# Optimization experiments

Hardware: AMD Instinct MI355X
Metric: run time of the kernel (lower is better)

Reference implementation:

```python
import jax, jax.numpy as jnp
import numpy as np

D_MODEL = 1024
NUM_HEADS = 16

def _dense_params(key, d_in, d_out):
    kw, _ = jax.random.split(key)
    # flax default: lecun_normal kernel, zeros bias
    W = jax.random.normal(kw, (d_in, d_out), dtype=jnp.float32) / np.sqrt(d_in)
    b = jnp.zeros((d_out,), dtype=jnp.float32)
    return W, b

def setup_inputs() -> dict:
    key = jax.random.key(0)
    ks = jax.random.split(key, 8)
    B, Tx, Tc = 2, 2048, 2048
    x = jax.random.normal(ks[0], (B, Tx, D_MODEL), dtype=jnp.float32)
    context = jax.random.normal(ks[1], (B, Tc, D_MODEL), dtype=jnp.float32)
    Wq, bq = _dense_params(ks[2], D_MODEL, D_MODEL)
    Wks, bks = _dense_params(ks[3], D_MODEL, D_MODEL)
    Wvs, bvs = _dense_params(ks[4], D_MODEL, D_MODEL)
    Wkc, bkc = _dense_params(ks[5], D_MODEL, D_MODEL)
    Wvc, bvc = _dense_params(ks[6], D_MODEL, D_MODEL)
    Wo, bo = _dense_params(ks[7], D_MODEL, D_MODEL)
    return {"x": x, "context": context,
            "Wq": Wq, "bq": bq, "Wks": Wks, "bks": bks, "Wvs": Wvs, "bvs": bvs,
            "Wkc": Wkc, "bkc": bkc, "Wvc": Wvc, "bvc": bvc, "Wo": Wo, "bo": bo}

def _split_heads(t, H):
    B, T, C = t.shape
    return t.reshape(B, T, H, C // H).transpose(0, 2, 1, 3)  # [B,H,T,hd]

def reference(x, context, Wq, bq, Wks, bks, Wvs, bvs, Wkc, bkc, Wvc, bvc, Wo, bo):
    H = NUM_HEADS
    head_dim = D_MODEL // H
    q = x @ Wq + bq
    k = jnp.concatenate([x @ Wks + bks, context @ Wkc + bkc], axis=1)
    v = jnp.concatenate([x @ Wvs + bvs, context @ Wvc + bvc], axis=1)
    q = _split_heads(q, H)  # [B,H,Tq,hd]
    k = _split_heads(k, H)  # [B,H,Tk,hd]
    v = _split_heads(v, H)
    attn = jnp.einsum('bhqd,bhkd->bhqk', q, k) / jnp.sqrt(jnp.float32(head_dim))
    attn = jax.nn.softmax(attn, axis=-1)
    out = jnp.einsum('bhqk,bhkd->bhqd', attn, v)
    B, _, Tq, _ = out.shape
    out = out.transpose(0, 2, 1, 3).reshape(B, Tq, D_MODEL)
    return out @ Wo + bo
```

## Files before the change

### kernel.cpp

```cpp
#include <hip/hip_runtime.h>
#include <hip/hip_bf16.h>
#include <math.h>


typedef _Float16 f16;
typedef _Float16 f16x8 __attribute__((ext_vector_type(8)));
typedef _Float16 f16x4v __attribute__((ext_vector_type(4)));
typedef float    f32x4 __attribute__((ext_vector_type(4)));

#define MFMA_F16(a, b, c) __builtin_amdgcn_mfma_f32_16x16x32_f16((a), (b), (c), 0, 0, 0)

#define QSCALE 0.18033688011112042f

__device__ __forceinline__ void glds16(const f16* g, f16* l) {
    __builtin_amdgcn_global_load_lds(
        (const __attribute__((address_space(1))) void*)g,
        (__attribute__((address_space(3))) void*)l, 16, 0, 0);
}

__global__ __launch_bounds__(256) void convert_xc(
    const float4* __restrict__ x, const float4* __restrict__ ctx,
    f16x4v* __restrict__ xb, f16x4v* __restrict__ cb)
{
    const int n4 = (2 * 2048 * 1024) / 4;
    int i = blockIdx.x * 256 + threadIdx.x;
    float4 v;
    f16x4v* dst;
    if (i < n4) { v = x[i];        dst = xb + i; }
    else        { v = ctx[i - n4]; dst = cb + (i - n4); }
    f16x4v h = { (f16)v.x, (f16)v.y, (f16)v.z, (f16)v.w };
    *dst = h;
}

__global__ __launch_bounds__(256) void pack_w(
    const float* __restrict__ W0, const float* __restrict__ W1,
    const float* __restrict__ W2, const float* __restrict__ W3,
    const float* __restrict__ W4, const float* __restrict__ W5,
    f16* __restrict__ out)
{
    const float* Ws[6] = { W0, W1, W2, W3, W4, W5 };
    const float* W = Ws[blockIdx.z];
    f16* Wt = out + (size_t)blockIdx.z * (1024 * 1024);

    __shared__ float tile[32][33];
    const int tx = threadIdx.x & 31, ty = threadIdx.x >> 5;
    const int n0 = blockIdx.x * 32, k0 = blockIdx.y * 32;

#pragma unroll
    for (int i = 0; i < 4; ++i) {
        int r = i * 8 + ty;
        tile[r][tx] = W[(size_t)(k0 + r) * 1024 + n0 + tx];
    }
    __syncthreads();
#pragma unroll
    for (int i = 0; i < 4; ++i) {
        int r = i * 8 + ty;
        Wt[(size_t)(n0 + r) * 1024 + k0 + tx] = (f16)tile[tx][r];
    }
}

#define GEMM_PROLOGUE(BN)                                                     \
    const int m0 = blockIdx.x * 128, n0 = blockIdx.y * (BN);                  \
    const int tid = threadIdx.x;                                              \
    const int w = tid >> 6, lane = tid & 63, quad = lane >> 4, l15 = lane & 15;\
    const int wm = (w >> 1) * 64, wn = (w & 1) * ((BN) / 2);                  \
    const int qsw = (quad ^ ((l15 >> 1) & 3)) * 8;                            \
    int gA[2], gB[(BN) / 64];                                                 \
    _Pragma("unroll")                                                         \
    for (int p = 0; p < 2; ++p) {                                             \
        int s = tid + p * 256;                                                \
        int r = (s >> 2) & 127, c = (s & 3) ^ ((s >> 3) & 3);                 \
        gA[p] = (m0 + r) * 1024 + c * 8;                                      \
    }                                                                         \
    _Pragma("unroll")                                                         \
    for (int p = 0; p < (BN) / 64; ++p) {                                     \
        int s = tid + p * 256;                                                \
        int r = (s >> 2) & ((BN) - 1), c = (s & 3) ^ ((s >> 3) & 3);          \
        gB[p] = (n0 + r) * 1024 + c * 8;                                      \
    }

#define GEMM_STAGE(BN)                                                        \
    __syncthreads();                                                          \
    _Pragma("unroll")                                                         \
    for (int p = 0; p < 2; ++p) glds16(&A[gA[p] + k0], &As[(p * 256 + w * 64) * 8]); \
    _Pragma("unroll")                                                         \
    for (int p = 0; p < (BN) / 64; ++p) glds16(&Bt[gB[p] + k0], &Bs[(p * 256 + w * 64) * 8]); \
    __syncthreads();

__global__ __launch_bounds__(256) void qk_gemm(
    const f16* __restrict__ xb, const f16* __restrict__ cb,
    const f16* __restrict__ wt,
    const float* __restrict__ bq, const float* __restrict__ bks,
    const float* __restrict__ bkc,
    f16* __restrict__ qbuf, f16* __restrict__ kbuf)
{
    __shared__ alignas(16) f16 As[128 * 32];
    __shared__ alignas(16) f16 Bs[128 * 32];

    const int z = blockIdx.z;
    const f16* A = (z == 2) ? cb : xb;
    const f16* Bt = wt + (size_t)(z == 0 ? 0 : (z == 1 ? 1 : 3)) * 1048576;
    const float* bias = (z == 0) ? bq : (z == 1) ? bks : bkc;
    const int roff = (z == 2) ? 2048 : 0;

    GEMM_PROLOGUE(128)
    f32x4 acc[4][4] = {};

    for (int k0 = 0; k0 < 1024; k0 += 32) {
        GEMM_STAGE(128)
        f16x8 a[4], b[4];
#pragma unroll
        for (int i = 0; i < 4; ++i)
            a[i] = *(const f16x8*)&As[(wm + i * 16 + l15) * 32 + qsw];
#pragma unroll
        for (int i = 0; i < 4; ++i)
            b[i] = *(const f16x8*)&Bs[(wn + i * 16 + l15) * 32 + qsw];
#pragma unroll
        for (int mi = 0; mi < 4; ++mi)
#pragma unroll
            for (int ni = 0; ni < 4; ++ni)
                acc[mi][ni] = MFMA_F16(a[mi], b[ni], acc[mi][ni]);
    }

#pragma unroll
    for (int mi = 0; mi < 4; ++mi) {
#pragma unroll
        for (int r = 0; r < 4; ++r) {
            int row = m0 + wm + mi * 16 + quad * 4 + r;
            int b_ = row >> 11, tok = row & 2047;
#pragma unroll
            for (int ni = 0; ni < 4; ++ni) {
                int col = n0 + wn + ni * 16 + l15;
                float v = acc[mi][ni][r] + bias[col];
                int bh = b_ * 16 + (col >> 6);
                if (z == 0) {
                    qbuf[((size_t)bh * 2048 + tok) * 64 + (col & 63)] = (f16)(v * QSCALE);
                } else {
                    int tg = roff + tok;
                    kbuf[(size_t)bh * 262144 + (size_t)(tg >> 6) * 4096
                         + (size_t)((col >> 5) & 1) * 2048 + (tg & 63) * 32 + (col & 31)] = (f16)v;
                }
            }
        }
    }
}

__global__ __launch_bounds__(256) void v_gemm(
    const f16* __restrict__ xb, const f16* __restrict__ cb,
    const f16* __restrict__ wt,
    const float* __restrict__ bvs, const float* __restrict__ bvc,
    f16* __restrict__ vt)
{
    __shared__ alignas(16) f16 As[128 * 32];
    __shared__ alignas(16) f16 Bs[128 * 32];

    const int z = blockIdx.z;
    const f16* A = z ? cb : xb;
    const f16* Bt = wt + (size_t)(z ? 4 : 2) * 1048576;
    const float* bias = z ? bvc : bvs;
    const int roff = z ? 2048 : 0;

    GEMM_PROLOGUE(128)
    f32x4 acc[4][4] = {};

    for (int k0 = 0; k0 < 1024; k0 += 32) {
        GEMM_STAGE(128)
        f16x8 a[4], b[4];
#pragma unroll
        for (int i = 0; i < 4; ++i)
            a[i] = *(const f16x8*)&As[(wm + i * 16 + l15) * 32 + qsw];
#pragma unroll
        for (int i = 0; i < 4; ++i)
            b[i] = *(const f16x8*)&Bs[(wn + i * 16 + l15) * 32 + qsw];
#pragma unroll
        for (int mi = 0; mi < 4; ++mi)
#pragma unroll
            for (int ni = 0; ni < 4; ++ni)
                acc[mi][ni] = MFMA_F16(b[ni], a[mi], acc[mi][ni]);
    }

#pragma unroll
    for (int mi = 0; mi < 4; ++mi) {
        int tok = m0 + wm + mi * 16 + l15;
        int b_ = tok >> 11;
        int tg = roff + (tok & 2047);
        size_t tbase = (size_t)(tg >> 6) * 4096 + (size_t)((tg >> 5) & 1) * 2048 + (tg & 31);
#pragma unroll
        for (int ni = 0; ni < 4; ++ni) {
#pragma unroll
            for (int r = 0; r < 4; ++r) {
                int wcol = n0 + wn + ni * 16 + quad * 4 + r;
                float v = acc[mi][ni][r] + bias[wcol];
                int bh = b_ * 16 + (wcol >> 6);
                vt[(size_t)bh * 262144 + tbase + (size_t)(wcol & 63) * 32] = (f16)v;
            }
        }
    }
}

__global__ __launch_bounds__(256) void out_gemm(
    const f16* __restrict__ abuf, const f16* __restrict__ wt5,
    const float* __restrict__ bo, float* __restrict__ out)
{
    __shared__ alignas(16) f16 As[128 * 32];
    __shared__ alignas(16) f16 Bs[64 * 32];

    const f16* A = abuf;
    const f16* Bt = wt5;

    GEMM_PROLOGUE(64)
    f32x4 acc[4][2] = {};

    for (int k0 = 0; k0 < 1024; k0 += 32) {
        GEMM_STAGE(64)
        f16x8 a[4], b[2];
#pragma unroll
        for (int i = 0; i < 4; ++i)
            a[i] = *(const f16x8*)&As[(wm + i * 16 + l15) * 32 + qsw];
#pragma unroll
        for (int i = 0; i < 2; ++i)
            b[i] = *(const f16x8*)&Bs[(wn + i * 16 + l15) * 32 + qsw];
#pragma unroll
        for (int mi = 0; mi < 4; ++mi)
#pragma unroll
            for (int ni = 0; ni < 2; ++ni)
                acc[mi][ni] = MFMA_F16(a[mi], b[ni], acc[mi][ni]);
    }

#pragma unroll
    for (int mi = 0; mi < 4; ++mi) {
#pragma unroll
        for (int r = 0; r < 4; ++r) {
            int row = m0 + wm + mi * 16 + quad * 4 + r;
#pragma unroll
            for (int ni = 0; ni < 2; ++ni) {
                int col = n0 + wn + ni * 16 + l15;
                out[(size_t)row * 1024 + col] = acc[mi][ni][r] + bo[col];
            }
        }
    }
}

__global__ __launch_bounds__(256, 2) void attn_kernel(
    const f16* __restrict__ q, const f16* __restrict__ kb,
    const f16* __restrict__ vtb, f16* __restrict__ o)
{
    __shared__ alignas(16) f16 K_lds[2][4096];
    __shared__ alignas(16) f16 V_lds[2][4096];
    __shared__ alignas(16) f16 P_lds[128 * 72];

    const int tid = threadIdx.x;
    const int w = tid >> 6, lane = tid & 63, quad = lane >> 4, l15 = lane & 15;
    const int bh = blockIdx.x, qt = blockIdx.y;
    const int b = bh >> 4, h = bh & 15;
    const int qbase = qt * 128;

    f16x8 qa[2][2];
#pragma unroll
    for (int nq = 0; nq < 2; ++nq) {
        const size_t qaddr =
            ((size_t)bh * 2048 + qbase + w * 32 + nq * 16 + l15) * 64 + quad * 8;
        qa[nq][0] = *(const f16x8*)&q[qaddr];
        qa[nq][1] = *(const f16x8*)&q[qaddr + 32];
    }

    f16x8 ones;
#pragma unroll
    for (int j = 0; j < 8; ++j) ones[j] = (f16)1.0f;

    f32x4 o_acc[2][4] = {};
    f32x4 l_acc[2] = {};

    const f16* ktile = kb + (size_t)bh * 262144;
    const f16* vtile = vtb + (size_t)bh * 262144;

    const int sco = ((tid >> 2) * 4 + ((tid & 3) ^ ((tid >> 3) & 3))) * 8;
    const int qsw = (quad ^ ((l15 >> 1) & 3)) * 8;
    const int wslot = w * 512;

    glds16(ktile + sco,        &K_lds[0][wslot]);
    glds16(ktile + 2048 + sco, &K_lds[0][2048 + wslot]);
    glds16(vtile + sco,        &V_lds[0][wslot]);
    glds16(vtile + 2048 + sco, &V_lds[0][2048 + wslot]);

    for (int kt = 0; kt < 64; ++kt) {
        const f16* Kc = K_lds[kt & 1];
        const f16* Vc = V_lds[kt & 1];
        f16* Kn = K_lds[(kt + 1) & 1];
        f16* Vn = V_lds[(kt + 1) & 1];

        __syncthreads();

        ktile += 4096; vtile += 4096;
        glds16(ktile + sco,        Kn + wslot);
        glds16(ktile + 2048 + sco, Kn + 2048 + wslot);
        glds16(vtile + sco,        Vn + wslot);
        glds16(vtile + 2048 + sco, Vn + 2048 + wslot);

        f32x4 s[4][2];
#pragma unroll
        for (int mt = 0; mt < 4; ++mt) {
            f16x8 ka0 = *(const f16x8*)&Kc[(mt * 16 + l15) * 32 + qsw];
            f16x8 ka1 = *(const f16x8*)&Kc[2048 + (mt * 16 + l15) * 32 + qsw];
#pragma unroll
            for (int nq = 0; nq < 2; ++nq) {
                f32x4 t = {};
                t = MFMA_F16(ka0, qa[nq][0], t);
                t = MFMA_F16(ka1, qa[nq][1], t);
                s[mt][nq] = t;
            }
        }

#pragma unroll
        for (int mt = 0; mt < 4; ++mt) {
#pragma unroll
            for (int nq = 0; nq < 2; ++nq) {
                f16x4v pk;
#pragma unroll
                for (int r = 0; r < 4; ++r)
                    pk[r] = (f16)__builtin_amdgcn_exp2f(s[mt][nq][r]);
                *(f16x4v*)&P_lds[(w * 32 + nq * 16 + l15) * 72 + mt * 16 + quad * 4] = pk;
            }
        }

        f16x8 pa[2][2];
#pragma unroll
        for (int nq = 0; nq < 2; ++nq)
#pragma unroll
            for (int ks = 0; ks < 2; ++ks)
                pa[nq][ks] = *(const f16x8*)&P_lds[(w * 32 + nq * 16 + l15) * 72 + ks * 32 + quad * 8];

#pragma unroll
        for (int nq = 0; nq < 2; ++nq) {
            l_acc[nq] = MFMA_F16(ones, pa[nq][0], l_acc[nq]);
            l_acc[nq] = MFMA_F16(ones, pa[nq][1], l_acc[nq]);
        }

#pragma unroll
        for (int dt = 0; dt < 4; ++dt) {
            f16x8 vb0 = *(const f16x8*)&Vc[(dt * 16 + l15) * 32 + qsw];
            f16x8 vb1 = *(const f16x8*)&Vc[2048 + (dt * 16 + l15) * 32 + qsw];
#pragma unroll
            for (int nq = 0; nq < 2; ++nq) {
                o_acc[nq][dt] = MFMA_F16(pa[nq][0], vb0, o_acc[nq][dt]);
                o_acc[nq][dt] = MFMA_F16(pa[nq][1], vb1, o_acc[nq][dt]);
            }
        }
    }

#pragma unroll
    for (int nq = 0; nq < 2; ++nq) {
#pragma unroll
        for (int r = 0; r < 4; ++r) {
            float lr = __shfl(l_acc[nq][0], quad * 4 + r, 64);
            float inv = 1.0f / lr;
            int ql = w * 32 + nq * 16 + quad * 4 + r;
            size_t obase = ((size_t)(b * 2048 + qbase + ql)) * 1024 + h * 64;
#pragma unroll
            for (int dt = 0; dt < 4; ++dt)
                o[obase + dt * 16 + l15] = (f16)(o_acc[nq][dt][r] * inv);
        }
    }
}

extern "C" void kernel_launch(void* const* d_in, const int* in_sizes, int n_in,
                              void* d_out, int out_size, void* d_ws, size_t ws_size,
                              hipStream_t stream)
{
    (void)in_sizes; (void)n_in; (void)out_size; (void)ws_size;

    const float* x    = (const float*)d_in[0];
    const float* ctx  = (const float*)d_in[1];
    const float* Wq   = (const float*)d_in[2];  const float* bq  = (const float*)d_in[3];
    const float* Wks  = (const float*)d_in[4];  const float* bks = (const float*)d_in[5];
    const float* Wvs  = (const float*)d_in[6];  const float* bvs = (const float*)d_in[7];
    const float* Wkc  = (const float*)d_in[8];  const float* bkc = (const float*)d_in[9];
    const float* Wvc  = (const float*)d_in[10]; const float* bvc = (const float*)d_in[11];
    const float* Wo   = (const float*)d_in[12]; const float* bo  = (const float*)d_in[13];

    char* ws = (char*)d_ws;
    f16* xb   = (f16*)(ws + 0);
    f16* cb   = (f16*)(ws + 8388608);
    f16* wt   = (f16*)(ws + 16777216);
    f16* qbuf = (f16*)(ws + 29360128);
    f16* kbuf = (f16*)(ws + 37748736);
    f16* vt   = (f16*)(ws + 54525952);
    f16* abuf = (f16*)(ws + 71303168);

    convert_xc<<<8192, 256, 0, stream>>>((const float4*)x, (const float4*)ctx,
                                         (f16x4v*)xb, (f16x4v*)cb);
    pack_w<<<dim3(32, 32, 6), 256, 0, stream>>>(Wq, Wks, Wvs, Wkc, Wvc, Wo, wt);

    qk_gemm<<<dim3(32, 8, 3), 256, 0, stream>>>(xb, cb, wt, bq, bks, bkc, qbuf, kbuf);
    v_gemm<<<dim3(32, 8, 2), 256, 0, stream>>>(xb, cb, wt, bvs, bvc, vt);

    attn_kernel<<<dim3(32, 16), 256, 0, stream>>>(qbuf, kbuf, vt, abuf);

    out_gemm<<<dim3(32, 16), 256, 0, stream>>>(abuf, wt + 5 * 1048576, bo, (float*)d_out);
}
```

Baseline: 317.8 us.

## Merge prep and projection kernels, add V transpose pass, widen attention waves

Fuses the input conversion and weight packing into one launch, and folds the Q/K and V projections into a single five-slice GEMM launch. V is now written row-major and transposed into the attention layout by a separate pass, reusing the xb workspace. The attention kernel drops to 128 threads per block, with each wave handling 64 queries instead of 32, which doubles register accumulators per wave and halves the number of waves. This trades launch count and occupancy for more K/V reuse per wave, at the cost of an extra V transpose kernel and higher register pressure.

After: 362.6 us. +14.1%, slower.

```diff
diff --git a/kernel.cpp b/kernel.cpp
--- a/kernel.cpp
+++ b/kernel.cpp
@@ -18,33 +18,34 @@
         (__attribute__((address_space(3))) void*)l, 16, 0, 0);
 }
 
-__global__ __launch_bounds__(256) void convert_xc(
+__global__ __launch_bounds__(256) void prep(
     const float4* __restrict__ x, const float4* __restrict__ ctx,
-    f16x4v* __restrict__ xb, f16x4v* __restrict__ cb)
-{
-    const int n4 = (2 * 2048 * 1024) / 4;
-    int i = blockIdx.x * 256 + threadIdx.x;
-    float4 v;
-    f16x4v* dst;
-    if (i < n4) { v = x[i];        dst = xb + i; }
-    else        { v = ctx[i - n4]; dst = cb + (i - n4); }
-    f16x4v h = { (f16)v.x, (f16)v.y, (f16)v.z, (f16)v.w };
-    *dst = h;
-}
-
-__global__ __launch_bounds__(256) void pack_w(
+    f16x4v* __restrict__ xb, f16x4v* __restrict__ cb,
     const float* __restrict__ W0, const float* __restrict__ W1,
     const float* __restrict__ W2, const float* __restrict__ W3,
     const float* __restrict__ W4, const float* __restrict__ W5,
-    f16* __restrict__ out)
-{
+    f16* __restrict__ wt)
+{
+    if (blockIdx.x < 8192) {
+        const int n4 = (2 * 2048 * 1024) / 4;
+        int i = blockIdx.x * 256 + threadIdx.x;
+        float4 v;
+        f16x4v* dst;
+        if (i < n4) { v = x[i];        dst = xb + i; }
+        else        { v = ctx[i - n4]; dst = cb + (i - n4); }
+        f16x4v h = { (f16)v.x, (f16)v.y, (f16)v.z, (f16)v.w };
+        *dst = h;
+        return;
+    }
+    const int idx = blockIdx.x - 8192;
+    const int z = idx >> 10, rem = idx & 1023;
     const float* Ws[6] = { W0, W1, W2, W3, W4, W5 };
-    const float* W = Ws[blockIdx.z];
-    f16* Wt = out + (size_t)blockIdx.z * (1024 * 1024);
+    const float* W = Ws[z];
+    f16* Wt = wt + (size_t)z * (1024 * 1024);
 
     __shared__ float tile[32][33];
     const int tx = threadIdx.x & 31, ty = threadIdx.x >> 5;
-    const int n0 = blockIdx.x * 32, k0 = blockIdx.y * 32;
+    const int n0 = (rem & 31) * 32, k0 = (rem >> 5) * 32;
 
 #pragma unroll
     for (int i = 0; i < 4; ++i) {
@@ -87,21 +88,24 @@
     for (int p = 0; p < (BN) / 64; ++p) glds16(&Bt[gB[p] + k0], &Bs[(p * 256 + w * 64) * 8]); \
     __syncthreads();
 
-__global__ __launch_bounds__(256) void qk_gemm(
+__global__ __launch_bounds__(256) void proj_gemm(
     const f16* __restrict__ xb, const f16* __restrict__ cb,
     const f16* __restrict__ wt,
     const float* __restrict__ bq, const float* __restrict__ bks,
-    const float* __restrict__ bkc,
-    f16* __restrict__ qbuf, f16* __restrict__ kbuf)
+    const float* __restrict__ bkc, const float* __restrict__ bvs,
+    const float* __restrict__ bvc,
+    f16* __restrict__ qbuf, f16* __restrict__ kbuf, f16* __restrict__ vbuf)
 {
     __shared__ alignas(16) f16 As[128 * 32];
     __shared__ alignas(16) f16 Bs[128 * 32];
 
     const int z = blockIdx.z;
-    const f16* A = (z == 2) ? cb : xb;
-    const f16* Bt = wt + (size_t)(z == 0 ? 0 : (z == 1 ? 1 : 3)) * 1048576;
-    const float* bias = (z == 0) ? bq : (z == 1) ? bks : bkc;
-    const int roff = (z == 2) ? 2048 : 0;
+    const f16* A = (z == 0 || z == 1 || z == 3) ? xb : cb;
+    const int wslot = (z == 0) ? 0 : (z == 1) ? 1 : (z == 2) ? 3 : (z == 3) ? 2 : 4;
+    const f16* Bt = wt + (size_t)wslot * 1048576;
+    const float* bias = (z == 0) ? bq : (z == 1) ? bks : (z == 2) ? bkc
+                        : (z == 3) ? bvs : bvc;
+    const int roff = (z == 2 || z == 4) ? 2048 : 0;
 
     GEMM_PROLOGUE(128)
     f32x4 acc[4][4] = {};
@@ -133,121 +137,50 @@
                 int col = n0 + wn + ni * 16 + l15;
                 float v = acc[mi][ni][r] + bias[col];
                 int bh = b_ * 16 + (col >> 6);
+                int tg = roff + tok;
                 if (z == 0) {
                     qbuf[((size_t)bh * 2048 + tok) * 64 + (col & 63)] = (f16)(v * QSCALE);
-                } else {
-                    int tg = roff + tok;
+                } else if (z <= 2) {
                     kbuf[(size_t)bh * 262144 + (size_t)(tg >> 6) * 4096
                          + (size_t)((col >> 5) & 1) * 2048 + (tg & 63) * 32 + (col & 31)] = (f16)v;
+                } else {
+                    vbuf[(size_t)bh * 262144 + (size_t)tg * 64 + (col & 63)] = (f16)v;
                 }
             }
         }
     }
 }
 
-__global__ __launch_bounds__(256) void v_gemm(
-    const f16* __restrict__ xb, const f16* __restrict__ cb,
-    const f16* __restrict__ wt,
-    const float* __restrict__ bvs, const float* __restrict__ bvc,
-    f16* __restrict__ vt)
-{
-    __shared__ alignas(16) f16 As[128 * 32];
-    __shared__ alignas(16) f16 Bs[128 * 32];
-
-    const int z = blockIdx.z;
-    const f16* A = z ? cb : xb;
-    const f16* Bt = wt + (size_t)(z ? 4 : 2) * 1048576;
-    const float* bias = z ? bvc : bvs;
-    const int roff = z ? 2048 : 0;
-
-    GEMM_PROLOGUE(128)
-    f32x4 acc[4][4] = {};
-
-    for (int k0 = 0; k0 < 1024; k0 += 32) {
-        GEMM_STAGE(128)
-        f16x8 a[4], b[4];
-#pragma unroll
-        for (int i = 0; i < 4; ++i)
-            a[i] = *(const f16x8*)&As[(wm + i * 16 + l15) * 32 + qsw];
-#pragma unroll
-        for (int i = 0; i < 4; ++i)
-            b[i] = *(const f16x8*)&Bs[(wn + i * 16 + l15) * 32 + qsw];
-#pragma unroll
-        for (int mi = 0; mi < 4; ++mi)
-#pragma unroll
-            for (int ni = 0; ni < 4; ++ni)
-                acc[mi][ni] = MFMA_F16(b[ni], a[mi], acc[mi][ni]);
-    }
-
-#pragma unroll
-    for (int mi = 0; mi < 4; ++mi) {
-        int tok = m0 + wm + mi * 16 + l15;
-        int b_ = tok >> 11;
-        int tg = roff + (tok & 2047);
-        size_t tbase = (size_t)(tg >> 6) * 4096 + (size_t)((tg >> 5) & 1) * 2048 + (tg & 31);
-#pragma unroll
-        for (int ni = 0; ni < 4; ++ni) {
-#pragma unroll
-            for (int r = 0; r < 4; ++r) {
-                int wcol = n0 + wn + ni * 16 + quad * 4 + r;
-                float v = acc[mi][ni][r] + bias[wcol];
-                int bh = b_ * 16 + (wcol >> 6);
-                vt[(size_t)bh * 262144 + tbase + (size_t)(wcol & 63) * 32] = (f16)v;
-            }
-        }
-    }
-}
-
-__global__ __launch_bounds__(256) void out_gemm(
-    const f16* __restrict__ abuf, const f16* __restrict__ wt5,
-    const float* __restrict__ bo, float* __restrict__ out)
-{
-    __shared__ alignas(16) f16 As[128 * 32];
-    __shared__ alignas(16) f16 Bs[64 * 32];
-
-    const f16* A = abuf;
-    const f16* Bt = wt5;
-
-    GEMM_PROLOGUE(64)
-    f32x4 acc[4][2] = {};
-
-    for (int k0 = 0; k0 < 1024; k0 += 32) {
-        GEMM_STAGE(64)
-        f16x8 a[4], b[2];
-#pragma unroll
-        for (int i = 0; i < 4; ++i)
-            a[i] = *(const f16x8*)&As[(wm + i * 16 + l15) * 32 + qsw];
-#pragma unroll
-        for (int i = 0; i < 2; ++i)
-            b[i] = *(const f16x8*)&Bs[(wn + i * 16 + l15) * 32 + qsw];
-#pragma unroll
-        for (int mi = 0; mi < 4; ++mi)
-#pragma unroll
-            for (int ni = 0; ni < 2; ++ni)
-                acc[mi][ni] = MFMA_F16(a[mi], b[ni], acc[mi][ni]);
-    }
-
-#pragma unroll
-    for (int mi = 0; mi < 4; ++mi) {
-#pragma unroll
-        for (int r = 0; r < 4; ++r) {
-            int row = m0 + wm + mi * 16 + quad * 4 + r;
-#pragma unroll
-            for (int ni = 0; ni < 2; ++ni) {
-                int col = n0 + wn + ni * 16 + l15;
-                out[(size_t)row * 1024 + col] = acc[mi][ni][r] + bo[col];
-            }
-        }
-    }
-}
-
-__global__ __launch_bounds__(256, 2) void attn_kernel(
+__global__ __launch_bounds__(256) void transpose_v(
+    const f16* __restrict__ vbuf, f16* __restrict__ vt)
+{
+    const int t = threadIdx.x;
+    const int mt = t >> 3, md = t & 7;
+    const int tok0 = blockIdx.x * 256 + mt * 8;
+    const int z = blockIdx.y;
+    f16x8 in[8];
+#pragma unroll
+    for (int i = 0; i < 8; ++i)
+        in[i] = *(const f16x8*)&vbuf[((size_t)z * 4096 + tok0 + i) * 64 + md * 8];
+    f16x8 ov[8];
+#pragma unroll
+    for (int j = 0; j < 8; ++j)
+#pragma unroll
+        for (int i = 0; i < 8; ++i) ov[j][i] = in[i][j];
+    const int kt = tok0 >> 6, kks = (tok0 >> 5) & 1, kko = tok0 & 31;
+#pragma unroll
+    for (int j = 0; j < 8; ++j)
+        *(f16x8*)&vt[(size_t)z * 262144 + (size_t)kt * 4096 + kks * 2048
+                     + (md * 8 + j) * 32 + kko] = ov[j];
+}
+
+__global__ __launch_bounds__(128) void attn_kernel(
     const f16* __restrict__ q, const f16* __restrict__ kb,
     const f16* __restrict__ vtb, f16* __restrict__ o)
 {
     __shared__ alignas(16) f16 K_lds[2][4096];
     __shared__ alignas(16) f16 V_lds[2][4096];
-    __shared__ alignas(16) f16 P_lds[128 * 72];
+    __shared__ alignas(16) f16 P_lds[2][64 * 72];
 
     const int tid = threadIdx.x;
     const int w = tid >> 6, lane = tid & 63, quad = lane >> 4, l15 = lane & 15;
@@ -255,11 +188,11 @@
     const int b = bh >> 4, h = bh & 15;
     const int qbase = qt * 128;
 
-    f16x8 qa[2][2];
-#pragma unroll
-    for (int nq = 0; nq < 2; ++nq) {
+    f16x8 qa[4][2];
+#pragma unroll
+    for (int nq = 0; nq < 4; ++nq) {
         const size_t qaddr =
-            ((size_t)bh * 2048 + qbase + w * 32 + nq * 16 + l15) * 64 + quad * 8;
+            ((size_t)bh * 2048 + qbase + w * 64 + nq * 16 + l15) * 64 + quad * 8;
         qa[nq][0] = *(const f16x8*)&q[qaddr];
         qa[nq][1] = *(const f16x8*)&q[qaddr + 32];
     }
@@ -268,20 +201,26 @@
 #pragma unroll
     for (int j = 0; j < 8; ++j) ones[j] = (f16)1.0f;
 
-    f32x4 o_acc[2][4] = {};
-    f32x4 l_acc[2] = {};
+    f32x4 o_acc[4][4] = {};
+    f32x4 l_acc[4] = {};
 
     const f16* ktile = kb + (size_t)bh * 262144;
     const f16* vtile = vtb + (size_t)bh * 262144;
 
-    const int sco = ((tid >> 2) * 4 + ((tid & 3) ^ ((tid >> 3) & 3))) * 8;
+    int goff[4];
+#pragma unroll
+    for (int p = 0; p < 4; ++p) {
+        int c = p * 128 + tid;
+        goff[p] = (c >> 2) * 32 + (((c & 3) ^ ((c >> 3) & 3)) * 8);
+    }
     const int qsw = (quad ^ ((l15 >> 1) & 3)) * 8;
-    const int wslot = w * 512;
-
-    glds16(ktile + sco,        &K_lds[0][wslot]);
-    glds16(ktile + 2048 + sco, &K_lds[0][2048 + wslot]);
-    glds16(vtile + sco,        &V_lds[0][wslot]);
-    glds16(vtile + 2048 + sco, &V_lds[0][2048 + wslot]);
+    f16* Pw = &P_lds[w][0];
+
+#pragma unroll
+    for (int p = 0; p < 4; ++p) {
+        glds16(ktile + goff[p], &K_lds[0][(p * 128 + w * 64) * 8]);
+        glds16(vtile + goff[p], &V_lds[0][(p * 128 + w * 64) * 8]);
+    }
 
     for (int kt = 0; kt < 64; ++kt) {
         const f16* Kc = K_lds[kt & 1];
@@ -292,46 +231,43 @@
         __syncthreads();
 
         ktile += 4096; vtile += 4096;
-        glds16(ktile + sco,        Kn + wslot);
-        glds16(ktile + 2048 + sco, Kn + 2048 + wslot);
-        glds16(vtile + sco,        Vn + wslot);
-        glds16(vtile + 2048 + sco, Vn + 2048 + wslot);
-
-        f32x4 s[4][2];
+#pragma unroll
+        for (int p = 0; p < 4; ++p) {
+            glds16(ktile + goff[p], &Kn[(p * 128 + w * 64) * 8]);
+            glds16(vtile + goff[p], &Vn[(p * 128 + w * 64) * 8]);
+        }
+
 #pragma unroll
         for (int mt = 0; mt < 4; ++mt) {
             f16x8 ka0 = *(const f16x8*)&Kc[(mt * 16 + l15) * 32 + qsw];
             f16x8 ka1 = *(const f16x8*)&Kc[2048 + (mt * 16 + l15) * 32 + qsw];
-#pragma unroll
-            for (int nq = 0; nq < 2; ++nq) {
+            f32x4 s[4];
+#pragma unroll
+            for (int nq = 0; nq < 4; ++nq) {
                 f32x4 t = {};
                 t = MFMA_F16(ka0, qa[nq][0], t);
                 t = MFMA_F16(ka1, qa[nq][1], t);
-                s[mt][nq] = t;
-            }
-        }
-
-#pragma unroll
-        for (int mt = 0; mt < 4; ++mt) {
-#pragma unroll
-            for (int nq = 0; nq < 2; ++nq) {
+                s[nq] = t;
+            }
+#pragma unroll
+            for (int nq = 0; nq < 4; ++nq) {
                 f16x4v pk;
 #pragma unroll
                 for (int r = 0; r < 4; ++r)
-                    pk[r] = (f16)__builtin_amdgcn_exp2f(s[mt][nq][r]);
-                *(f16x4v*)&P_lds[(w * 32 + nq * 16 + l15) * 72 + mt * 16 + quad * 4] = pk;
-            }
-        }
-
-        f16x8 pa[2][2];
-#pragma unroll
-        for (int nq = 0; nq < 2; ++nq)
+                    pk[r] = (f16)__builtin_amdgcn_exp2f(s[nq][r]);
+                *(f16x4v*)&Pw[(nq * 16 + l15) * 72 + mt * 16 + quad * 4] = pk;
+            }
+        }
+
+        f16x8 pa[4][2];
+#pragma unroll
+        for (int nq = 0; nq < 4; ++nq)
 #pragma unroll
             for (int ks = 0; ks < 2; ++ks)
-                pa[nq][ks] = *(const f16x8*)&P_lds[(w * 32 + nq * 16 + l15) * 72 + ks * 32 + quad * 8];
-
-#pragma unroll
-        for (int nq = 0; nq < 2; ++nq) {
+                pa[nq][ks] = *(const f16x8*)&Pw[(nq * 16 + l15) * 72 + ks * 32 + quad * 8];
+
+#pragma unroll
+        for (int nq = 0; nq < 4; ++nq) {
             l_acc[nq] = MFMA_F16(ones, pa[nq][0], l_acc[nq]);
             l_acc[nq] = MFMA_F16(ones, pa[nq][1], l_acc[nq]);
         }
@@ -341,7 +277,7 @@
             f16x8 vb0 = *(const f16x8*)&Vc[(dt * 16 + l15) * 32 + qsw];
             f16x8 vb1 = *(const f16x8*)&Vc[2048 + (dt * 16 + l15) * 32 + qsw];
 #pragma unroll
-            for (int nq = 0; nq < 2; ++nq) {
+            for (int nq = 0; nq < 4; ++nq) {
                 o_acc[nq][dt] = MFMA_F16(pa[nq][0], vb0, o_acc[nq][dt]);
                 o_acc[nq][dt] = MFMA_F16(pa[nq][1], vb1, o_acc[nq][dt]);
             }
@@ -349,16 +285,59 @@
     }
 
 #pragma unroll
-    for (int nq = 0; nq < 2; ++nq) {
+    for (int nq = 0; nq < 4; ++nq) {
 #pragma unroll
         for (int r = 0; r < 4; ++r) {
             float lr = __shfl(l_acc[nq][0], quad * 4 + r, 64);
             float inv = 1.0f / lr;
-            int ql = w * 32 + nq * 16 + quad * 4 + r;
+            int ql = w * 64 + nq * 16 + quad * 4 + r;
             size_t obase = ((size_t)(b * 2048 + qbase + ql)) * 1024 + h * 64;
 #pragma unroll
             for (int dt = 0; dt < 4; ++dt)
                 o[obase + dt * 16 + l15] = (f16)(o_acc[nq][dt][r] * inv);
+        }
+    }
+}
+
+__global__ __launch_bounds__(256) void out_gemm(
+    const f16* __restrict__ abuf, const f16* __restrict__ wt5,
+    const float* __restrict__ bo, float* __restrict__ out)
+{
+    __shared__ alignas(16) f16 As[128 * 32];
+    __shared__ alignas(16) f16 Bs[64 * 32];
+
+    const f16* A = abuf;
+    const f16* Bt = wt5;
+
+    GEMM_PROLOGUE(64)
+    f32x4 acc[4][2] = {};
+
+    for (int k0 = 0; k0 < 1024; k0 += 32) {
+        GEMM_STAGE(64)
+        f16x8 a[4], b[2];
+#pragma unroll
+        for (int i = 0; i < 4; ++i)
+            a[i] = *(const f16x8*)&As[(wm + i * 16 + l15) * 32 + qsw];
+#pragma unroll
+        for (int i = 0; i < 2; ++i)
+            b[i] = *(const f16x8*)&Bs[(wn + i * 16 + l15) * 32 + qsw];
+#pragma unroll
+        for (int mi = 0; mi < 4; ++mi)
+#pragma unroll
+            for (int ni = 0; ni < 2; ++ni)
+                acc[mi][ni] = MFMA_F16(a[mi], b[ni], acc[mi][ni]);
+    }
+
+#pragma unroll
+    for (int mi = 0; mi < 4; ++mi) {
+#pragma unroll
+        for (int r = 0; r < 4; ++r) {
+            int row = m0 + wm + mi * 16 + quad * 4 + r;
+#pragma unroll
+            for (int ni = 0; ni < 2; ++ni) {
+                int col = n0 + wn + ni * 16 + l15;
+                out[(size_t)row * 1024 + col] = acc[mi][ni][r] + bo[col];
+            }
         }
     }
 }
@@ -381,20 +360,23 @@
     char* ws = (char*)d_ws;
     f16* xb   = (f16*)(ws + 0);
     f16* cb   = (f16*)(ws + 8388608);
+    f16* vt   = (f16*)(ws + 0);
     f16* wt   = (f16*)(ws + 16777216);
     f16* qbuf = (f16*)(ws + 29360128);
     f16* kbuf = (f16*)(ws + 37748736);
-    f16* vt   = (f16*)(ws + 54525952);
+    f16* vbuf = (f16*)(ws + 54525952);
     f16* abuf = (f16*)(ws + 71303168);
 
-    convert_xc<<<8192, 256, 0, stream>>>((const float4*)x, (const float4*)ctx,
-                                         (f16x4v*)xb, (f16x4v*)cb);
-    pack_w<<<dim3(32, 32, 6), 256, 0, stream>>>(Wq, Wks, Wvs, Wkc, Wvc, Wo, wt);
-
-    qk_gemm<<<dim3(32, 8, 3), 256, 0, stream>>>(xb, cb, wt, bq, bks, bkc, qbuf, kbuf);
-    v_gemm<<<dim3(32, 8, 2), 256, 0, stream>>>(xb, cb, wt, bvs, bvc, vt);
-
-    attn_kernel<<<dim3(32, 16), 256, 0, stream>>>(qbuf, kbuf, vt, abuf);
+    prep<<<14336, 256, 0, stream>>>((const float4*)x, (const float4*)ctx,
+                                    (f16x4v*)xb, (f16x4v*)cb,
+                                    Wq, Wks, Wvs, Wkc, Wvc, Wo, wt);
+
+    proj_gemm<<<dim3(32, 8, 5), 256, 0, stream>>>(
+        xb, cb, wt, bq, bks, bkc, bvs, bvc, qbuf, kbuf, vbuf);
+
+    transpose_v<<<dim3(16, 32), 256, 0, stream>>>(vbuf, vt);
+
+    attn_kernel<<<dim3(32, 16), 128, 0, stream>>>(qbuf, kbuf, vt, abuf);
 
     out_gemm<<<dim3(32, 16), 256, 0, stream>>>(abuf, wt + 5 * 1048576, bo, (float*)d_out);
 }
```
